# Kernel tuning notes

Hardware: AMD Instinct MI355X
Metric: run time of the kernel (lower is better)

## Reference

```python
import jax, jax.numpy as jnp
import numpy as np

DIM = 512
HEADS = 8


def setup_inputs() -> dict:
    key = jax.random.key(0)
    ks = jax.random.split(key, 8)
    B, N_mm, N_a, N_v = 2, 64, 256, 256
    xmm = jax.random.normal(ks[0], (B, N_mm, DIM), dtype=jnp.float32)
    xa = jax.random.normal(ks[1], (B, N_a, DIM), dtype=jnp.float32)
    xv = jax.random.normal(ks[2], (B, N_v, DIM), dtype=jnp.float32)
    # Learned params (torch nn.Linear stores weight as [out, in]); qkv_bias=False, proj has bias.
    Wq = jax.random.normal(ks[3], (DIM, DIM), dtype=jnp.float32) * 0.02
    Wkv = jax.random.normal(ks[4], (2 * DIM, 2 * DIM), dtype=jnp.float32) * 0.02
    Wproj = jax.random.normal(ks[5], (DIM, DIM), dtype=jnp.float32) * 0.02
    bproj = jnp.zeros((DIM,), dtype=jnp.float32)
    return {"xmm": xmm, "xa": xa, "xv": xv, "Wq": Wq, "Wkv": Wkv, "Wproj": Wproj, "bproj": bproj}


def reference(xmm, xa, xv, Wq, Wkv, Wproj, bproj):
    B, N_mm, dim = xmm.shape
    N_v, N_a = xv.shape[1], xa.shape[1]
    H = HEADS
    hd = dim // H
    scale = hd ** (-0.5)

    # q: [B, H, N_mm, hd]
    q = (xmm @ Wq.T).reshape(B, N_mm, H, hd).transpose(0, 2, 1, 3)

    # kv(x_va) where x_va[b,i,j] = concat(xv[b,i], xa[b,j]); since kv is linear,
    # kv(x_va) = xv @ Wkv[:, :dim].T + xa @ Wkv[:, dim:].T, broadcast over the cartesian grid.
    pv = xv @ Wkv[:, :dim].T   # [B, N_v, 2*dim]
    pa = xa @ Wkv[:, dim:].T   # [B, N_a, 2*dim]
    kv = (pv[:, :, None, :] + pa[:, None, :, :]).reshape(B, N_v * N_a, 2, H, hd)
    k = kv[:, :, 0].transpose(0, 2, 1, 3)  # [B, H, N_v*N_a, hd]
    v = kv[:, :, 1].transpose(0, 2, 1, 3)  # [B, H, N_v*N_a, hd]

    attn = jax.nn.softmax(jnp.einsum('bhqd,bhkd->bhqk', q, k) * scale, axis=-1)
    out = jnp.einsum('bhqk,bhkd->bhqd', attn, v)          # [B, H, N_mm, hd]
    out = out.transpose(0, 2, 1, 3).reshape(B, N_mm, dim)  # [B, N_mm, dim]
    return out @ Wproj.T + bproj
```

## Files before the change

kernel.cpp:

```cpp
#include <hip/hip_runtime.h>


#define OQ16   0
#define OK16   65536
#define OVT16  589824
#define SIDESZ 262144
#define OHOUT16 1114112

typedef _Float16 f16x8 __attribute__((ext_vector_type(8)));
typedef _Float16 f16x4 __attribute__((ext_vector_type(4)));
typedef float f32x4 __attribute__((ext_vector_type(4)));

__device__ __forceinline__ void stage_tile_f16(
    const float* __restrict__ g, const float* __restrict__ g2, int ld,
    int base, int k0, _Float16* __restrict__ lds, int sr, int sq)
{
  const float* p = &g[(size_t)(base + sr) * ld + k0 + sq * 16];
  float4 v0 = *reinterpret_cast<const float4*>(p);
  float4 v1 = *reinterpret_cast<const float4*>(p + 4);
  float4 v2 = *reinterpret_cast<const float4*>(p + 8);
  float4 v3 = *reinterpret_cast<const float4*>(p + 12);
  if (g2) {
    const float* p2 = &g2[(size_t)(base + sr) * ld + k0 + sq * 16];
    float4 u0 = *reinterpret_cast<const float4*>(p2);
    float4 u1 = *reinterpret_cast<const float4*>(p2 + 4);
    float4 u2 = *reinterpret_cast<const float4*>(p2 + 8);
    float4 u3 = *reinterpret_cast<const float4*>(p2 + 12);
    v0.x += u0.x; v0.y += u0.y; v0.z += u0.z; v0.w += u0.w;
    v1.x += u1.x; v1.y += u1.y; v1.z += u1.z; v1.w += u1.w;
    v2.x += u2.x; v2.y += u2.y; v2.z += u2.z; v2.w += u2.w;
    v3.x += u3.x; v3.y += u3.y; v3.z += u3.z; v3.w += u3.w;
  }
  f16x8 h0 = {(_Float16)v0.x, (_Float16)v0.y, (_Float16)v0.z, (_Float16)v0.w,
              (_Float16)v1.x, (_Float16)v1.y, (_Float16)v1.z, (_Float16)v1.w};
  f16x8 h1 = {(_Float16)v2.x, (_Float16)v2.y, (_Float16)v2.z, (_Float16)v2.w,
              (_Float16)v3.x, (_Float16)v3.y, (_Float16)v3.z, (_Float16)v3.w};
  int c0 = (sq * 2) ^ (sr & 7);
  int c1 = (sq * 2 + 1) ^ (sr & 7);
  *reinterpret_cast<f16x8*>(&lds[sr * 64 + c0 * 8]) = h0;
  *reinterpret_cast<f16x8*>(&lds[sr * 64 + c1 * 8]) = h1;
}

template <int MODE>
__device__ __forceinline__ void mfma_gemm64(
    const float* __restrict__ A, const float* __restrict__ A2, int lda,
    const float* __restrict__ W, int ldw,
    int bm, int bn, int side,
    _Float16* __restrict__ ws16,
    float* __restrict__ Cf, int ldc, const float* __restrict__ bias)
{
  __shared__ _Float16 As[64 * 64];
  __shared__ _Float16 Ws[64 * 64];
  const int tid = threadIdx.x;
  const int lane = tid & 63;
  const int w = tid >> 6;
  const int wm = w >> 1, wn = w & 1;
  const int sr = tid >> 2;
  const int sq = tid & 3;

  f32x4 acc[2][2] = {};
  const int cl = lane & 15;
  const int kg = lane >> 4;

  for (int k0 = 0; k0 < 512; k0 += 64) {
    __syncthreads();
    stage_tile_f16(A, A2, lda, bm, k0, As, sr, sq);
    stage_tile_f16(W, nullptr, ldw, bn, k0, Ws, sr, sq);
    __syncthreads();
    #pragma unroll
    for (int ks = 0; ks < 2; ++ks) {
      f16x8 af[2], bf[2];
      #pragma unroll
      for (int mi = 0; mi < 2; ++mi) {
        int row = wm * 32 + mi * 16 + cl;
        int ch = (ks * 4 + kg) ^ (row & 7);
        af[mi] = *reinterpret_cast<const f16x8*>(&As[row * 64 + ch * 8]);
      }
      #pragma unroll
      for (int ni = 0; ni < 2; ++ni) {
        int col = wn * 32 + ni * 16 + cl;
        int ch = (ks * 4 + kg) ^ (col & 7);
        bf[ni] = *reinterpret_cast<const f16x8*>(&Ws[col * 64 + ch * 8]);
      }
      #pragma unroll
      for (int mi = 0; mi < 2; ++mi)
        #pragma unroll
        for (int ni = 0; ni < 2; ++ni)
          acc[mi][ni] = __builtin_amdgcn_mfma_f32_16x16x32_f16(
              af[mi], bf[ni], acc[mi][ni], 0, 0, 0);
    }
  }

  #pragma unroll
  for (int mi = 0; mi < 2; ++mi) {
    #pragma unroll
    for (int ni = 0; ni < 2; ++ni) {
      int row0 = bm + wm * 32 + mi * 16 + kg * 4;
      int col = bn + wn * 32 + ni * 16 + cl;
      if (MODE == 0) {
        int b = row0 >> 6, n = row0 & 63, h = col >> 6, d = col & 63;
        _Float16* dst = ws16 + OQ16 + (((size_t)b * 8 + h) * 64 + n) * 64 + d;
        #pragma unroll
        for (int r = 0; r < 4; ++r)
          dst[(size_t)r * 64] = (_Float16)(acc[mi][ni][r] * 0.125f);
      } else if (MODE == 1) {
        int b = row0 >> 8, key = row0 & 255;
        if (col < 512) {
          int h = col >> 6, d = col & 63;
          _Float16* dst = ws16 + OK16 + (size_t)side * SIDESZ +
                          (((size_t)b * 8 + h) * 256 + key) * 64 + d;
          #pragma unroll
          for (int r = 0; r < 4; ++r)
            dst[(size_t)r * 64] = (_Float16)acc[mi][ni][r];
        } else {
          int dp = col - 512;
          int h = dp >> 6, d = dp & 63;
          _Float16* dst = ws16 + OVT16 + (size_t)side * SIDESZ +
                          (((size_t)b * 8 + h) * 64 + d) * 256 + key;
          f16x4 v = {(_Float16)acc[mi][ni][0], (_Float16)acc[mi][ni][1],
                     (_Float16)acc[mi][ni][2], (_Float16)acc[mi][ni][3]};
          *reinterpret_cast<f16x4*>(dst) = v;
        }
      } else {
        float bv = bias ? bias[col] : 0.f;
        #pragma unroll
        for (int r = 0; r < 4; ++r)
          Cf[(size_t)(row0 + r) * ldc + col] = acc[mi][ni][r] + bv;
      }
    }
  }
}

__global__ __launch_bounds__(256) void fused_proj_kernel(
    const float* __restrict__ xmm, const float* __restrict__ xa,
    const float* __restrict__ xv, const float* __restrict__ Wq,
    const float* __restrict__ Wkv, _Float16* __restrict__ ws16)
{
  const int id = blockIdx.x;
  if (id < 16) {
    mfma_gemm64<0>(xmm, nullptr, 512, Wq, 512, (id >> 3) * 64, (id & 7) * 64,
                   0, ws16, nullptr, 0, nullptr);
  } else if (id < 144) {
    int t = id - 16;
    mfma_gemm64<1>(xv, nullptr, 512, Wkv, 1024, (t >> 4) * 64, (t & 15) * 64,
                   0, ws16, nullptr, 0, nullptr);
  } else {
    int t = id - 144;
    mfma_gemm64<1>(xa, nullptr, 512, Wkv + 512, 1024, (t >> 4) * 64,
                   (t & 15) * 64, 1, ws16, nullptr, 0, nullptr);
  }
}

__global__ __launch_bounds__(256) void proj_out_kernel(
    const _Float16* __restrict__ ws16, const float* __restrict__ Wproj,
    const float* __restrict__ bproj, float* __restrict__ out)
{
  const float* hv = (const float*)(ws16 + OHOUT16);
  const float* ha = hv + 65536;
  mfma_gemm64<2>(hv, ha, 512, Wproj, 512,
                 (int)(blockIdx.x >> 3) * 64, (int)(blockIdx.x & 7) * 64, 0,
                 nullptr, out, 512, bproj);
}

__global__ __launch_bounds__(256) void attn_kernel(
    const _Float16* __restrict__ ws16, float* __restrict__ hv,
    float* __restrict__ ha)
{
  __shared__ _Float16 P_lds[16][256];
  __shared__ float m_s[4][16];
  __shared__ float l_s[4][16];

  const int x = blockIdx.x;
  const int side = x & 1;
  const int qtl = (x >> 1) & 3;
  const int bh = x >> 3;
  const int b = bh >> 3;

  const int tid = threadIdx.x;
  const int w = tid >> 6;
  const int lane = tid & 63;
  const int l15 = lane & 15;
  const int g = lane >> 4;

  const _Float16* slabQ = ws16 + OQ16 + (size_t)bh * 4096;
  const _Float16* slabK = ws16 + OK16 + (size_t)side * SIDESZ + (size_t)bh * 16384;
  const _Float16* slabV = ws16 + OVT16 + (size_t)side * SIDESZ + (size_t)bh * 16384;

  f16x8 qb[2];
  #pragma unroll
  for (int ks = 0; ks < 2; ++ks)
    qb[ks] = *reinterpret_cast<const f16x8*>(
        &slabQ[(size_t)(qtl * 16 + l15) * 64 + ks * 32 + g * 8]);

  f32x4 st[4] = {};
  #pragma unroll
  for (int f = 0; f < 4; ++f) {
    #pragma unroll
    for (int ks = 0; ks < 2; ++ks) {
      f16x8 af = *reinterpret_cast<const f16x8*>(
          &slabK[(size_t)(w * 64 + f * 16 + l15) * 64 + ks * 32 + g * 8]);
      st[f] = __builtin_amdgcn_mfma_f32_16x16x32_f16(af, qb[ks], st[f], 0, 0, 0);
    }
  }

  float m = st[0][0];
  #pragma unroll
  for (int f = 0; f < 4; ++f)
    #pragma unroll
    for (int r = 0; r < 4; ++r) m = fmaxf(m, st[f][r]);
  m = fmaxf(m, __shfl_xor(m, 16));
  m = fmaxf(m, __shfl_xor(m, 32));
  if (g == 0) m_s[w][l15] = m;
  __syncthreads();

  float M = fmaxf(fmaxf(m_s[0][l15], m_s[1][l15]),
                  fmaxf(m_s[2][l15], m_s[3][l15]));
  float lsum = 0.f;
  #pragma unroll
  for (int f = 0; f < 4; ++f)
    #pragma unroll
    for (int r = 0; r < 4; ++r) {
      float e = __expf(st[f][r] - M);
      st[f][r] = e;
      lsum += e;
    }
  lsum += __shfl_xor(lsum, 16);
  lsum += __shfl_xor(lsum, 32);
  if (g == 0) l_s[w][l15] = lsum;

  #pragma unroll
  for (int f = 0; f < 4; ++f) {
    f16x4 pk = {(_Float16)st[f][0], (_Float16)st[f][1],
                (_Float16)st[f][2], (_Float16)st[f][3]};
    int chunk = w * 8 + 2 * f + (g >> 1);
    int swz = chunk ^ (l15 & 7);
    *reinterpret_cast<f16x4*>(&P_lds[l15][swz * 8 + (g & 1) * 4]) = pk;
  }
  __syncthreads();

  f32x4 L4 = {};
  #pragma unroll
  for (int w2 = 0; w2 < 4; ++w2) {
    f32x4 lw = *reinterpret_cast<const f32x4*>(&l_s[w2][g * 4]);
    L4 += lw;
  }

  f32x4 oc = {};
  #pragma unroll
  for (int ks = 0; ks < 8; ++ks) {
    f16x8 pa = *reinterpret_cast<const f16x8*>(
        &P_lds[l15][((4 * ks + g) ^ (l15 & 7)) * 8]);
    f16x8 vb = *reinterpret_cast<const f16x8*>(
        &slabV[(size_t)(w * 16 + l15) * 256 + ks * 32 + g * 8]);
    oc = __builtin_amdgcn_mfma_f32_16x16x32_f16(pa, vb, oc, 0, 0, 0);
  }

  float* houtS = side ? ha : hv;
  const int h = bh & 7;
  #pragma unroll
  for (int r = 0; r < 4; ++r) {
    houtS[(size_t)(b * 64 + qtl * 16 + 4 * g + r) * 512 +
          h * 64 + w * 16 + l15] = oc[r] * (1.0f / L4[r]);
  }
}

extern "C" void kernel_launch(void* const* d_in, const int* in_sizes, int n_in,
                              void* d_out, int out_size, void* d_ws, size_t ws_size,
                              hipStream_t stream) {
  const float* xmm   = (const float*)d_in[0];
  const float* xa    = (const float*)d_in[1];
  const float* xv    = (const float*)d_in[2];
  const float* Wq    = (const float*)d_in[3];
  const float* Wkv   = (const float*)d_in[4];
  const float* Wproj = (const float*)d_in[5];
  const float* bproj = (const float*)d_in[6];
  float* out = (float*)d_out;
  _Float16* ws16 = (_Float16*)d_ws;
  float* hv = (float*)(ws16 + OHOUT16);
  float* ha = hv + 65536;

  fused_proj_kernel<<<272, 256, 0, stream>>>(xmm, xa, xv, Wq, Wkv, ws16);
  attn_kernel<<<128, 256, 0, stream>>>(ws16, hv, ha);
  proj_out_kernel<<<16, 256, 0, stream>>>(ws16, Wproj, bproj, out);
}
```

Before: 37.04 us.

## Fuse projection, attention and output GEMM into one persistent kernel with grid barriers

Replaces the three separate launches with a single 256-block kernel that runs the QKV projections, then attention, then the output projection, separated by atomic-counter grid barriers in workspace. The 272 projection tiles are spread over 256 blocks, so 16 blocks take two tiles. The intent is to remove inter-kernel launch gaps and drain time. The cost is an extra memset, spin-wait barriers, and co-residency assumptions for all 256 blocks, plus idle blocks during the attention and output stages.

```diff
diff --git a/kernel.cpp b/kernel.cpp
--- a/kernel.cpp
+++ b/kernel.cpp
@@ -6,10 +6,26 @@
 #define OVT16  589824
 #define SIDESZ 262144
 #define OHOUT16 1114112
+#define BAR_BYTE_OFF (4u << 20)
+#define NBLK 256
 
 typedef _Float16 f16x8 __attribute__((ext_vector_type(8)));
 typedef _Float16 f16x4 __attribute__((ext_vector_type(4)));
 typedef float f32x4 __attribute__((ext_vector_type(4)));
+
+__device__ __forceinline__ void gbar(int* cnt)
+{
+  __syncthreads();
+  if (threadIdx.x == 0) {
+    __threadfence();
+    __hip_atomic_fetch_add(cnt, 1, __ATOMIC_RELEASE, __HIP_MEMORY_SCOPE_AGENT);
+    while (__hip_atomic_load(cnt, __ATOMIC_ACQUIRE,
+                             __HIP_MEMORY_SCOPE_AGENT) < NBLK)
+      __builtin_amdgcn_s_sleep(1);
+    __threadfence();
+  }
+  __syncthreads();
+}
 
 __device__ __forceinline__ void stage_tile_f16(
     const float* __restrict__ g, const float* __restrict__ g2, int ld,
@@ -42,15 +58,14 @@
 }
 
 template <int MODE>
-__device__ __forceinline__ void mfma_gemm64(
+__device__ void gemm_task(
     const float* __restrict__ A, const float* __restrict__ A2, int lda,
     const float* __restrict__ W, int ldw,
     int bm, int bn, int side,
     _Float16* __restrict__ ws16,
-    float* __restrict__ Cf, int ldc, const float* __restrict__ bias)
-{
-  __shared__ _Float16 As[64 * 64];
-  __shared__ _Float16 Ws[64 * 64];
+    float* __restrict__ Cf, int ldc, const float* __restrict__ bias,
+    _Float16* __restrict__ As, _Float16* __restrict__ Ws)
+{
   const int tid = threadIdx.x;
   const int lane = tid & 63;
   const int w = tid >> 6;
@@ -131,46 +146,14 @@
   }
 }
 
-__global__ __launch_bounds__(256) void fused_proj_kernel(
-    const float* __restrict__ xmm, const float* __restrict__ xa,
-    const float* __restrict__ xv, const float* __restrict__ Wq,
-    const float* __restrict__ Wkv, _Float16* __restrict__ ws16)
-{
-  const int id = blockIdx.x;
-  if (id < 16) {
-    mfma_gemm64<0>(xmm, nullptr, 512, Wq, 512, (id >> 3) * 64, (id & 7) * 64,
-                   0, ws16, nullptr, 0, nullptr);
-  } else if (id < 144) {
-    int t = id - 16;
-    mfma_gemm64<1>(xv, nullptr, 512, Wkv, 1024, (t >> 4) * 64, (t & 15) * 64,
-                   0, ws16, nullptr, 0, nullptr);
-  } else {
-    int t = id - 144;
-    mfma_gemm64<1>(xa, nullptr, 512, Wkv + 512, 1024, (t >> 4) * 64,
-                   (t & 15) * 64, 1, ws16, nullptr, 0, nullptr);
-  }
-}
-
-__global__ __launch_bounds__(256) void proj_out_kernel(
-    const _Float16* __restrict__ ws16, const float* __restrict__ Wproj,
-    const float* __restrict__ bproj, float* __restrict__ out)
-{
-  const float* hv = (const float*)(ws16 + OHOUT16);
-  const float* ha = hv + 65536;
-  mfma_gemm64<2>(hv, ha, 512, Wproj, 512,
-                 (int)(blockIdx.x >> 3) * 64, (int)(blockIdx.x & 7) * 64, 0,
-                 nullptr, out, 512, bproj);
-}
-
-__global__ __launch_bounds__(256) void attn_kernel(
+__device__ void attn_task(
     const _Float16* __restrict__ ws16, float* __restrict__ hv,
-    float* __restrict__ ha)
-{
-  __shared__ _Float16 P_lds[16][256];
-  __shared__ float m_s[4][16];
-  __shared__ float l_s[4][16];
-
-  const int x = blockIdx.x;
+    float* __restrict__ ha, int x, _Float16* __restrict__ smem)
+{
+  _Float16* P = smem;
+  float* m_s = (float*)(smem + 4096);
+  float* l_s = m_s + 64;
+
   const int side = x & 1;
   const int qtl = (x >> 1) & 3;
   const int bh = x >> 3;
@@ -210,11 +193,11 @@
     for (int r = 0; r < 4; ++r) m = fmaxf(m, st[f][r]);
   m = fmaxf(m, __shfl_xor(m, 16));
   m = fmaxf(m, __shfl_xor(m, 32));
-  if (g == 0) m_s[w][l15] = m;
-  __syncthreads();
-
-  float M = fmaxf(fmaxf(m_s[0][l15], m_s[1][l15]),
-                  fmaxf(m_s[2][l15], m_s[3][l15]));
+  if (g == 0) m_s[w * 16 + l15] = m;
+  __syncthreads();
+
+  float M = fmaxf(fmaxf(m_s[l15], m_s[16 + l15]),
+                  fmaxf(m_s[32 + l15], m_s[48 + l15]));
   float lsum = 0.f;
   #pragma unroll
   for (int f = 0; f < 4; ++f)
@@ -226,7 +209,7 @@
     }
   lsum += __shfl_xor(lsum, 16);
   lsum += __shfl_xor(lsum, 32);
-  if (g == 0) l_s[w][l15] = lsum;
+  if (g == 0) l_s[w * 16 + l15] = lsum;
 
   #pragma unroll
   for (int f = 0; f < 4; ++f) {
@@ -234,22 +217,20 @@
                 (_Float16)st[f][2], (_Float16)st[f][3]};
     int chunk = w * 8 + 2 * f + (g >> 1);
     int swz = chunk ^ (l15 & 7);
-    *reinterpret_cast<f16x4*>(&P_lds[l15][swz * 8 + (g & 1) * 4]) = pk;
+    *reinterpret_cast<f16x4*>(&P[l15 * 256 + swz * 8 + (g & 1) * 4]) = pk;
   }
   __syncthreads();
 
   f32x4 L4 = {};
   #pragma unroll
-  for (int w2 = 0; w2 < 4; ++w2) {
-    f32x4 lw = *reinterpret_cast<const f32x4*>(&l_s[w2][g * 4]);
-    L4 += lw;
-  }
+  for (int w2 = 0; w2 < 4; ++w2)
+    L4 += *reinterpret_cast<const f32x4*>(&l_s[w2 * 16 + g * 4]);
 
   f32x4 oc = {};
   #pragma unroll
   for (int ks = 0; ks < 8; ++ks) {
     f16x8 pa = *reinterpret_cast<const f16x8*>(
-        &P_lds[l15][((4 * ks + g) ^ (l15 & 7)) * 8]);
+        &P[l15 * 256 + ((4 * ks + g) ^ (l15 & 7)) * 8]);
     f16x8 vb = *reinterpret_cast<const f16x8*>(
         &slabV[(size_t)(w * 16 + l15) * 256 + ks * 32 + g * 8]);
     oc = __builtin_amdgcn_mfma_f32_16x16x32_f16(pa, vb, oc, 0, 0, 0);
@@ -258,9 +239,55 @@
   float* houtS = side ? ha : hv;
   const int h = bh & 7;
   #pragma unroll
-  for (int r = 0; r < 4; ++r) {
+  for (int r = 0; r < 4; ++r)
     houtS[(size_t)(b * 64 + qtl * 16 + 4 * g + r) * 512 +
           h * 64 + w * 16 + l15] = oc[r] * (1.0f / L4[r]);
+  __syncthreads();
+}
+
+__global__ __launch_bounds__(256) void fused_all_kernel(
+    const float* __restrict__ xmm, const float* __restrict__ xa,
+    const float* __restrict__ xv, const float* __restrict__ Wq,
+    const float* __restrict__ Wkv, const float* __restrict__ Wproj,
+    const float* __restrict__ bproj, float* __restrict__ out,
+    _Float16* __restrict__ ws16, int* __restrict__ bar)
+{
+  __shared__ __align__(16) _Float16 smem[8448];
+  _Float16* As = smem;
+  _Float16* Ws = smem + 4096;
+  const int bid = blockIdx.x;
+
+  {
+    int t = bid;
+    if (t < 16) {
+      gemm_task<0>(xmm, nullptr, 512, Wq, 512, (t >> 3) * 64, (t & 7) * 64, 0,
+                   ws16, nullptr, 0, nullptr, As, Ws);
+    } else if (t < 144) {
+      int u = t - 16;
+      gemm_task<1>(xv, nullptr, 512, Wkv, 1024, (u >> 4) * 64, (u & 15) * 64,
+                   0, ws16, nullptr, 0, nullptr, As, Ws);
+    } else {
+      int u = t - 144;
+      gemm_task<1>(xa, nullptr, 512, Wkv + 512, 1024, (u >> 4) * 64,
+                   (u & 15) * 64, 1, ws16, nullptr, 0, nullptr, As, Ws);
+    }
+    if (bid >= 240) {
+      int u = bid - 240 + 112;
+      gemm_task<1>(xa, nullptr, 512, Wkv + 512, 1024, (u >> 4) * 64,
+                   (u & 15) * 64, 1, ws16, nullptr, 0, nullptr, As, Ws);
+    }
+  }
+  gbar(bar);
+
+  float* hv = (float*)(ws16 + OHOUT16);
+  float* ha = hv + 65536;
+  if (bid < 128) attn_task(ws16, hv, ha, bid, smem);
+  gbar(bar + 1);
+
+  if (bid >= 128 && bid < 144) {
+    int t = bid - 128;
+    gemm_task<2>(hv, ha, 512, Wproj, 512, (t >> 3) * 64, (t & 7) * 64, 0,
+                 nullptr, out, 512, bproj, As, Ws);
   }
 }
 
@@ -276,10 +303,9 @@
   const float* bproj = (const float*)d_in[6];
   float* out = (float*)d_out;
   _Float16* ws16 = (_Float16*)d_ws;
-  float* hv = (float*)(ws16 + OHOUT16);
-  float* ha = hv + 65536;
-
-  fused_proj_kernel<<<272, 256, 0, stream>>>(xmm, xa, xv, Wq, Wkv, ws16);
-  attn_kernel<<<128, 256, 0, stream>>>(ws16, hv, ha);
-  proj_out_kernel<<<16, 256, 0, stream>>>(ws16, Wproj, bproj, out);
-}
+  int* bar = (int*)((char*)d_ws + BAR_BYTE_OFF);
+
+  hipMemsetAsync(bar, 0, 16, stream);
+  fused_all_kernel<<<NBLK, 256, 0, stream>>>(
+      xmm, xa, xv, Wq, Wkv, Wproj, bproj, out, ws16, bar);
+}
```

After: 132.8 us. +258.5%, slower.

## Process all 64 queries per block with K/V/Q staged in swizzled LDS

Applied to the files above, without the earlier changes.

Restructures the attention kernel so that each block of 512 threads handles all 64 queries for one (batch, head, side). K, V and Q are loaded cooperatively into XOR-swizzled shared memory instead of being read from global memory four times, once per query tile. The grid shrinks from 128 blocks to 32, which cuts redundant K/V traffic but leaves far fewer blocks to spread across the GPU's compute units. It also adds extra barriers for the block-wide max and sum reductions.

```diff
diff --git a/kernel.cpp b/kernel.cpp
--- a/kernel.cpp
+++ b/kernel.cpp
@@ -162,106 +162,165 @@
                  nullptr, out, 512, bproj);
 }
 
-__global__ __launch_bounds__(256) void attn_kernel(
+__global__ __launch_bounds__(512) void attn_kernel(
     const _Float16* __restrict__ ws16, float* __restrict__ hv,
     float* __restrict__ ha)
 {
-  __shared__ _Float16 P_lds[16][256];
-  __shared__ float m_s[4][16];
-  __shared__ float l_s[4][16];
+  __shared__ __align__(16) _Float16 smem[55552];
+  _Float16* Kl = smem;
+  _Float16* Vl = smem + 16384;
+  _Float16* Ql = smem + 32768;
+  _Float16* P  = smem + 36864;
+  float* m_s  = (float*)(smem + 53248);
+  float* l_s  = m_s + 512;
+  float* Mtot = l_s + 512;
+  float* Ltot = Mtot + 64;
 
   const int x = blockIdx.x;
   const int side = x & 1;
-  const int qtl = (x >> 1) & 3;
-  const int bh = x >> 3;
-  const int b = bh >> 3;
+  const int bh = x >> 1;
+  const int b = bh >> 3, h = bh & 7;
 
   const int tid = threadIdx.x;
   const int w = tid >> 6;
   const int lane = tid & 63;
   const int l15 = lane & 15;
-  const int g = lane >> 4;
-
-  const _Float16* slabQ = ws16 + OQ16 + (size_t)bh * 4096;
-  const _Float16* slabK = ws16 + OK16 + (size_t)side * SIDESZ + (size_t)bh * 16384;
-  const _Float16* slabV = ws16 + OVT16 + (size_t)side * SIDESZ + (size_t)bh * 16384;
-
-  f16x8 qb[2];
-  #pragma unroll
-  for (int ks = 0; ks < 2; ++ks)
-    qb[ks] = *reinterpret_cast<const f16x8*>(
-        &slabQ[(size_t)(qtl * 16 + l15) * 64 + ks * 32 + g * 8]);
-
-  f32x4 st[4] = {};
-  #pragma unroll
-  for (int f = 0; f < 4; ++f) {
+  const int kg = lane >> 4;
+
+  const _Float16* gQ = ws16 + OQ16 + (size_t)bh * 4096;
+  const _Float16* gK = ws16 + OK16 + (size_t)side * SIDESZ + (size_t)bh * 16384;
+  const _Float16* gV = ws16 + OVT16 + (size_t)side * SIDESZ + (size_t)bh * 16384;
+
+  {
+    int ch = tid;
+    int row = ch >> 3, c = ch & 7;
+    *reinterpret_cast<f16x8*>(&Ql[row * 64 + ((c ^ (row & 7)) * 8)]) =
+        *reinterpret_cast<const f16x8*>(&gQ[ch * 8]);
+  }
+  #pragma unroll
+  for (int i = 0; i < 4; ++i) {
+    int ch = tid + i * 512;
+    int row = ch >> 3, c = ch & 7;
+    *reinterpret_cast<f16x8*>(&Kl[row * 64 + ((c ^ (row & 7)) * 8)]) =
+        *reinterpret_cast<const f16x8*>(&gK[ch * 8]);
+  }
+  #pragma unroll
+  for (int i = 0; i < 4; ++i) {
+    int ch = tid + i * 512;
+    int row = ch >> 5, c = ch & 31;
+    *reinterpret_cast<f16x8*>(&Vl[row * 256 + ((c ^ (row & 7)) * 8)]) =
+        *reinterpret_cast<const f16x8*>(&gV[ch * 8]);
+  }
+  __syncthreads();
+
+  f16x8 qb[4][2];
+  #pragma unroll
+  for (int qf = 0; qf < 4; ++qf)
+    #pragma unroll
+    for (int ks = 0; ks < 2; ++ks)
+      qb[qf][ks] = *reinterpret_cast<const f16x8*>(
+          &Ql[(qf * 16 + l15) * 64 + (((ks * 4 + kg) ^ (l15 & 7)) * 8)]);
+
+  f32x4 st[2][4] = {};
+  #pragma unroll
+  for (int kf = 0; kf < 2; ++kf) {
+    int krow = w * 32 + kf * 16 + l15;
     #pragma unroll
     for (int ks = 0; ks < 2; ++ks) {
       f16x8 af = *reinterpret_cast<const f16x8*>(
-          &slabK[(size_t)(w * 64 + f * 16 + l15) * 64 + ks * 32 + g * 8]);
-      st[f] = __builtin_amdgcn_mfma_f32_16x16x32_f16(af, qb[ks], st[f], 0, 0, 0);
-    }
-  }
-
-  float m = st[0][0];
-  #pragma unroll
-  for (int f = 0; f < 4; ++f)
-    #pragma unroll
-    for (int r = 0; r < 4; ++r) m = fmaxf(m, st[f][r]);
-  m = fmaxf(m, __shfl_xor(m, 16));
-  m = fmaxf(m, __shfl_xor(m, 32));
-  if (g == 0) m_s[w][l15] = m;
-  __syncthreads();
-
-  float M = fmaxf(fmaxf(m_s[0][l15], m_s[1][l15]),
-                  fmaxf(m_s[2][l15], m_s[3][l15]));
-  float lsum = 0.f;
-  #pragma unroll
-  for (int f = 0; f < 4; ++f)
-    #pragma unroll
-    for (int r = 0; r < 4; ++r) {
-      float e = __expf(st[f][r] - M);
-      st[f][r] = e;
-      lsum += e;
-    }
-  lsum += __shfl_xor(lsum, 16);
-  lsum += __shfl_xor(lsum, 32);
-  if (g == 0) l_s[w][l15] = lsum;
-
-  #pragma unroll
-  for (int f = 0; f < 4; ++f) {
-    f16x4 pk = {(_Float16)st[f][0], (_Float16)st[f][1],
-                (_Float16)st[f][2], (_Float16)st[f][3]};
-    int chunk = w * 8 + 2 * f + (g >> 1);
-    int swz = chunk ^ (l15 & 7);
-    *reinterpret_cast<f16x4*>(&P_lds[l15][swz * 8 + (g & 1) * 4]) = pk;
-  }
-  __syncthreads();
-
-  f32x4 L4 = {};
-  #pragma unroll
-  for (int w2 = 0; w2 < 4; ++w2) {
-    f32x4 lw = *reinterpret_cast<const f32x4*>(&l_s[w2][g * 4]);
-    L4 += lw;
-  }
-
-  f32x4 oc = {};
+          &Kl[krow * 64 + (((ks * 4 + kg) ^ (l15 & 7)) * 8)]);
+      #pragma unroll
+      for (int qf = 0; qf < 4; ++qf)
+        st[kf][qf] = __builtin_amdgcn_mfma_f32_16x16x32_f16(
+            af, qb[qf][ks], st[kf][qf], 0, 0, 0);
+    }
+  }
+
+  float mx[4];
+  #pragma unroll
+  for (int qf = 0; qf < 4; ++qf) {
+    float m = st[0][qf][0];
+    #pragma unroll
+    for (int kf = 0; kf < 2; ++kf)
+      #pragma unroll
+      for (int r = 0; r < 4; ++r) m = fmaxf(m, st[kf][qf][r]);
+    m = fmaxf(m, __shfl_xor(m, 16));
+    m = fmaxf(m, __shfl_xor(m, 32));
+    mx[qf] = m;
+  }
+  if (kg == 0) {
+    #pragma unroll
+    for (int qf = 0; qf < 4; ++qf) m_s[w * 64 + qf * 16 + l15] = mx[qf];
+  }
+  __syncthreads();
+  if (tid < 64) {
+    float M = m_s[tid];
+    #pragma unroll
+    for (int w2 = 1; w2 < 8; ++w2) M = fmaxf(M, m_s[w2 * 64 + tid]);
+    Mtot[tid] = M;
+  }
+  __syncthreads();
+
+  #pragma unroll
+  for (int qf = 0; qf < 4; ++qf) {
+    float M = Mtot[qf * 16 + l15];
+    float ls = 0.f;
+    #pragma unroll
+    for (int kf = 0; kf < 2; ++kf)
+      #pragma unroll
+      for (int r = 0; r < 4; ++r) {
+        float e = __expf(st[kf][qf][r] - M);
+        st[kf][qf][r] = e;
+        ls += e;
+      }
+    ls += __shfl_xor(ls, 16);
+    ls += __shfl_xor(ls, 32);
+    if (kg == 0) l_s[w * 64 + qf * 16 + l15] = ls;
+    #pragma unroll
+    for (int kf = 0; kf < 2; ++kf) {
+      int q = qf * 16 + l15;
+      int chunk = w * 4 + kf * 2 + (kg >> 1);
+      f16x4 pk = {(_Float16)st[kf][qf][0], (_Float16)st[kf][qf][1],
+                  (_Float16)st[kf][qf][2], (_Float16)st[kf][qf][3]};
+      *reinterpret_cast<f16x4*>(
+          &P[q * 256 + ((chunk ^ (q & 7)) * 8) + (kg & 1) * 4]) = pk;
+    }
+  }
+  __syncthreads();
+  if (tid < 64) {
+    float L = l_s[tid];
+    #pragma unroll
+    for (int w2 = 1; w2 < 8; ++w2) L += l_s[w2 * 64 + tid];
+    Ltot[tid] = L;
+  }
+  __syncthreads();
+
+  const int qf = w & 3;
+  const int d0 = (w >> 2) * 2;
+  f32x4 oc[2] = {};
   #pragma unroll
   for (int ks = 0; ks < 8; ++ks) {
     f16x8 pa = *reinterpret_cast<const f16x8*>(
-        &P_lds[l15][((4 * ks + g) ^ (l15 & 7)) * 8]);
-    f16x8 vb = *reinterpret_cast<const f16x8*>(
-        &slabV[(size_t)(w * 16 + l15) * 256 + ks * 32 + g * 8]);
-    oc = __builtin_amdgcn_mfma_f32_16x16x32_f16(pa, vb, oc, 0, 0, 0);
+        &P[(qf * 16 + l15) * 256 + (((ks * 4 + kg) ^ (l15 & 7)) * 8)]);
+    #pragma unroll
+    for (int j = 0; j < 2; ++j) {
+      int d = (d0 + j) * 16 + l15;
+      f16x8 vb = *reinterpret_cast<const f16x8*>(
+          &Vl[d * 256 + (((ks * 4 + kg) ^ (d & 7)) * 8)]);
+      oc[j] = __builtin_amdgcn_mfma_f32_16x16x32_f16(pa, vb, oc[j], 0, 0, 0);
+    }
   }
 
   float* houtS = side ? ha : hv;
-  const int h = bh & 7;
-  #pragma unroll
-  for (int r = 0; r < 4; ++r) {
-    houtS[(size_t)(b * 64 + qtl * 16 + 4 * g + r) * 512 +
-          h * 64 + w * 16 + l15] = oc[r] * (1.0f / L4[r]);
-  }
+  #pragma unroll
+  for (int j = 0; j < 2; ++j)
+    #pragma unroll
+    for (int r = 0; r < 4; ++r) {
+      int q = qf * 16 + kg * 4 + r;
+      int d = (d0 + j) * 16 + l15;
+      houtS[(size_t)(b * 64 + q) * 512 + h * 64 + d] =
+          oc[j][r] * (1.0f / Ltot[q]);
+    }
 }
 
 extern "C" void kernel_launch(void* const* d_in, const int* in_sizes, int n_in,
@@ -280,6 +339,6 @@
   float* ha = hv + 65536;
 
   fused_proj_kernel<<<272, 256, 0, stream>>>(xmm, xa, xv, Wq, Wkv, ws16);
-  attn_kernel<<<128, 256, 0, stream>>>(ws16, hv, ha);
+  attn_kernel<<<32, 512, 0, stream>>>(ws16, hv, ha);
   proj_out_kernel<<<16, 256, 0, stream>>>(ws16, Wproj, bproj, out);
 }
```

After: 34.56 us. -6.7%, faster.
